# Kernel optimization log

Measured on AMD Instinct MI355X. Metric: run time of the kernel, lower is better.

## Reference

```python
import jax, jax.numpy as jnp
import numpy as np

EMBED_DIM = 1024
NUM_HEADS = 16
HEAD_DIM = EMBED_DIM // NUM_HEADS


def setup_inputs() -> dict:
    key = jax.random.key(0)
    k_x, k_wqkv, k_bqkv, k_wo, k_bo = jax.random.split(key, 5)
    B, T, C = 4, 2048, EMBED_DIM
    # PyTorch Linear default init scale ~ 1/sqrt(fan_in); use small normals
    s = 1.0 / np.sqrt(C)
    return {
        "x": jax.random.normal(k_x, (B, T, C), dtype=jnp.float32),
        "w_qkv": jax.random.normal(k_wqkv, (C, 3 * C), dtype=jnp.float32) * s,
        "b_qkv": jax.random.normal(k_bqkv, (3 * C,), dtype=jnp.float32) * s,
        "w_out": jax.random.normal(k_wo, (C, C), dtype=jnp.float32) * s,
        "b_out": jax.random.normal(k_bo, (C,), dtype=jnp.float32) * s,
    }


def reference(x, w_qkv, b_qkv, w_out, b_out):
    B, T, C = x.shape
    H, D = NUM_HEADS, HEAD_DIM
    qkv = x @ w_qkv + b_qkv                      # (B, T, 3C)
    q, k, v = jnp.split(qkv, 3, axis=-1)
    # (B, H, T, D)
    q = q.reshape(B, T, H, D).transpose(0, 2, 1, 3)
    k = k.reshape(B, T, H, D).transpose(0, 2, 1, 3)
    v = v.reshape(B, T, H, D).transpose(0, 2, 1, 3)
    scores = jnp.einsum("bhqd,bhkd->bhqk", q, k) / jnp.sqrt(jnp.float32(D))
    causal = jnp.tril(jnp.ones((T, T), dtype=bool))  # (T, T)
    scores = jnp.where(causal[None, None, :, :], scores, -jnp.inf)
    attn = jax.nn.softmax(scores, axis=-1)
    out = jnp.einsum("bhqk,bhkd->bhqd", attn, v)  # (B, H, T, D)
    out = out.transpose(0, 2, 1, 3).reshape(B, T, C)
    return out @ w_out + b_out
```

## Files before the change

kernel.cpp:

```cpp
#include <hip/hip_runtime.h>
#include <hip/hip_bf16.h>

#define B_  4
#define T_  2048
#define C_  1024
#define H_  16
#define D_  64
#define BH_ (B_*H_)

typedef float  f32x4  __attribute__((ext_vector_type(4)));
typedef __bf16 bf16x8 __attribute__((ext_vector_type(8)));
typedef __bf16 bf16x2 __attribute__((ext_vector_type(2)));

static __device__ __forceinline__ ushort f2bf(float f) {
    union { float f; unsigned u; } x; x.f = f;
    unsigned r = ((x.u >> 16) & 1u) + 0x7fffu;
    return (ushort)((x.u + r) >> 16);
}

static __device__ __forceinline__ uint packbf(float a, float b) {
    bf16x2 v = { (__bf16)a, (__bf16)b };
    return __builtin_bit_cast(uint, v);
}

static __device__ __forceinline__ void gload_lds16(const void* g, void* l) {
    __builtin_amdgcn_global_load_lds(
        (const __attribute__((address_space(1))) unsigned int*)g,
        (__attribute__((address_space(3))) unsigned int*)l, 16, 0, 0);
}

template<int N> static __device__ __forceinline__ void waitcnt_vm() {
    if constexpr (N == 0) asm volatile("s_waitcnt vmcnt(0)" ::: "memory");
    else if constexpr (N == 3) asm volatile("s_waitcnt vmcnt(3)" ::: "memory");
    else if constexpr (N == 4) asm volatile("s_waitcnt vmcnt(4)" ::: "memory");
    else static_assert(N == 0 || N == 3 || N == 4);
    __builtin_amdgcn_sched_barrier(0);
}
static __device__ __forceinline__ void lgkm0() {
    asm volatile("s_waitcnt lgkmcnt(0)" ::: "memory");
    __builtin_amdgcn_sched_barrier(0);
}

__global__ void cvt_kernel(const float* __restrict__ in, ushort* __restrict__ out, int n) {
    int i = (blockIdx.x * blockDim.x + threadIdx.x) * 4;
    if (i < n) {
        float4 v = *(const float4*)(in + i);
        ushort4 o;
        o.x = f2bf(v.x); o.y = f2bf(v.y); o.z = f2bf(v.z); o.w = f2bf(v.w);
        *(ushort4*)(out + i) = o;
    }
}

__global__ void transpose_cvt_kernel(const float* __restrict__ in, ushort* __restrict__ out,
                                     int K, int N) {
    __shared__ float tile[32][33];
    int k0 = blockIdx.y * 32, n0 = blockIdx.x * 32;
    int tx = threadIdx.x & 31, ty = threadIdx.x >> 5;
    #pragma unroll
    for (int r = 0; r < 32; r += 8)
        tile[ty + r][tx] = in[(size_t)(k0 + ty + r) * N + n0 + tx];
    __syncthreads();
    #pragma unroll
    for (int r = 0; r < 32; r += 8)
        out[(size_t)(n0 + ty + r) * K + k0 + tx] = f2bf(tile[tx][ty + r]);
}

template<int MFR, int NFR, bool QKV>
__global__ __launch_bounds__(512, 2) void gemm_hk(
    const ushort* __restrict__ A,
    const ushort* __restrict__ Bt,
    const float*  __restrict__ bias,
    void* __restrict__ outp,
    ushort* __restrict__ vtp)
{
    constexpr int NT    = 16;
    constexpr int BM    = MFR * 32;
    constexpr int BN    = NFR * 64;
    constexpr int APASS = BM / 128;
    constexpr int LB    = BN / 128;
    constexpr int ABUF  = BM * 128;
    constexpr int BBUF  = BN * 128;
    constexpr int PK    = APASS + LB;
    __shared__ __align__(16) char lds[2 * ABUF + 2 * BBUF];
    char* ldsB = lds + 2 * ABUF;

    const int gX   = gridDim.x;
    const int orig = blockIdx.y * gX + blockIdx.x;
    const int cpx  = (gX * gridDim.y) >> 3;
    const int wg   = (orig & 7) * cpx + (orig >> 3);
    const int m0 = (wg / gX) * BM, n0 = (wg % gX) * BN;

    const int tid = threadIdx.x, lane = tid & 63;
    const int wv = tid >> 6, wm = wv >> 2, wn = wv & 3;
    const int lr = lane & 15, lh = lane >> 4;

    const int sc = (tid & 3) ^ ((tid >> 2) & 3);
    const ushort* aA = A  + (size_t)(m0 + (tid >> 2)) * 1024 + sc * 8;
    const ushort* aB = Bt + (size_t)(n0 + (tid >> 2)) * 1024 + sc * 8;

    const int cxor = (lh ^ (lr & 3)) * 16;
    const int arow = (wm * (MFR * 16) + lr) * 64 + cxor;
    const int brow = (wn * (NFR * 16) + lr) * 64 + cxor;

    f32x4 acc[MFR][NFR] = {};

    auto stage_a = [&](int buf, int t, int kh) {
        #pragma unroll
        for (int p = 0; p < APASS; ++p)
            gload_lds16(aA + (size_t)p * 131072 + t * 64 + kh * 32,
                        lds + buf * ABUF + kh * (ABUF / 2) + p * 8192 + tid * 16);
    };
    auto stage_b = [&](int buf, int t, int kh) {
        #pragma unroll
        for (int p = 0; p < LB; ++p)
            gload_lds16(aB + (size_t)p * 131072 + t * 64 + kh * 32,
                        ldsB + buf * BBUF + kh * (BBUF / 2) + p * 8192 + tid * 16);
    };
    auto read_a = [&](bf16x8 (&af)[MFR], int buf, int kh) {
        const char* base = lds + buf * ABUF + kh * (ABUF / 2) + arow;
        #pragma unroll
        for (int mi = 0; mi < MFR; ++mi) af[mi] = *(const bf16x8*)(base + mi * 1024);
    };
    auto read_b = [&](bf16x8& b0, bf16x8& b1, int buf, int kh, int nh) {
        const char* base = ldsB + buf * BBUF + kh * (BBUF / 2) + brow + nh * 2048;
        b0 = *(const bf16x8*)(base);
        b1 = *(const bf16x8*)(base + 1024);
    };

#define MFMA2(NI, BB0, BB1)                                                          \
    do {                                                                             \
        __builtin_amdgcn_s_setprio(1);                                               \
        _Pragma("unroll")                                                            \
        for (int mi = 0; mi < MFR; ++mi) {                                           \
            acc[mi][NI]     = __builtin_amdgcn_mfma_f32_16x16x32_bf16(af[mi], BB0,   \
                                                     acc[mi][NI], 0, 0, 0);          \
            acc[mi][NI + 1] = __builtin_amdgcn_mfma_f32_16x16x32_bf16(af[mi], BB1,   \
                                                     acc[mi][NI + 1], 0, 0, 0);      \
        }                                                                            \
        __builtin_amdgcn_s_setprio(0);                                               \
    } while (0)

    stage_a(0, 0, 0); stage_b(0, 0, 0);
    stage_a(0, 0, 1); stage_b(0, 0, 1);
    waitcnt_vm<PK>();
    __builtin_amdgcn_s_barrier();

    for (int t = 0; t < NT; ++t) {
        const int cur = t & 1, nxt = cur ^ 1;
        const bool pf = (t + 1 < NT);
        bf16x8 af[MFR], b0, b1;
        if constexpr (NFR == 4) {
            read_a(af, cur, 0); read_b(b0, b1, cur, 0, 0);
            if (pf) stage_a(nxt, t + 1, 0);
            __builtin_amdgcn_s_barrier();
            lgkm0();
            MFMA2(0, b0, b1);
            read_b(b0, b1, cur, 0, 1);
            if (pf) stage_b(nxt, t + 1, 0);
            if (t < NT - 1) waitcnt_vm<PK>(); else waitcnt_vm<0>();
            __builtin_amdgcn_s_barrier();
            lgkm0();
            MFMA2(2, b0, b1);
            read_a(af, cur, 1); read_b(b0, b1, cur, 1, 0);
            if (pf) stage_a(nxt, t + 1, 1);
            __builtin_amdgcn_s_barrier();
            lgkm0();
            MFMA2(0, b0, b1);
            read_b(b0, b1, cur, 1, 1);
            if (pf) stage_b(nxt, t + 1, 1);
            if (t < NT - 1) waitcnt_vm<PK>();
            __builtin_amdgcn_s_barrier();
            lgkm0();
            MFMA2(2, b0, b1);
        } else {
            read_a(af, cur, 0); read_b(b0, b1, cur, 0, 0);
            if (pf) { stage_a(nxt, t + 1, 0); stage_b(nxt, t + 1, 0); }
            if (t < NT - 1) waitcnt_vm<PK>(); else waitcnt_vm<0>();
            __builtin_amdgcn_s_barrier();
            lgkm0();
            MFMA2(0, b0, b1);
            read_a(af, cur, 1); read_b(b0, b1, cur, 1, 0);
            if (pf) { stage_a(nxt, t + 1, 1); stage_b(nxt, t + 1, 1); }
            if (t < NT - 1) waitcnt_vm<PK>();
            __builtin_amdgcn_s_barrier();
            lgkm0();
            MFMA2(0, b0, b1);
        }
    }
#undef MFMA2

    #pragma unroll
    for (int mi = 0; mi < MFR; ++mi) {
        #pragma unroll
        for (int ni = 0; ni < NFR; ++ni) {
            int col = n0 + wn * (NFR * 16) + ni * 16 + lr;
            float bv = bias[col];
            if constexpr (QKV) {
                ushort* qkv = (ushort*)outp;
                int which = col >> 10;
                int h = (col & 1023) >> 6;
                int d = col & 63;
                if (which == 2) {
                    #pragma unroll
                    for (int r = 0; r < 4; ++r) {
                        int row = m0 + wm * (MFR * 16) + mi * 16 + lh * 4 + r;
                        int b = row >> 11, tt = row & 2047;
                        vtp[(((size_t)(b * H_ + h)) * D_ + d) * T_ + tt] =
                            f2bf(acc[mi][ni][r] + bv);
                    }
                } else {
                    #pragma unroll
                    for (int r = 0; r < 4; ++r) {
                        int row = m0 + wm * (MFR * 16) + mi * 16 + lh * 4 + r;
                        int b = row >> 11, tt = row & 2047;
                        float v = acc[mi][ni][r] + bv;
                        if (which == 0) v *= 0.18033688011112042f;
                        qkv[(size_t)which * (BH_ * T_ * D_) +
                            (((size_t)(b * H_ + h)) * T_ + tt) * D_ + d] = f2bf(v);
                    }
                }
            } else {
                float* Cout = (float*)outp;
                #pragma unroll
                for (int r = 0; r < 4; ++r) {
                    int row = m0 + wm * (MFR * 16) + mi * 16 + lh * 4 + r;
                    Cout[(size_t)row * C_ + col] = acc[mi][ni][r] + bv;
                }
            }
        }
    }
}

__global__ __launch_bounds__(256, 5) void flash_kernel(
    const ushort* __restrict__ qb,
    const ushort* __restrict__ kb,
    const ushort* __restrict__ vt,
    ushort* __restrict__ ob)
{
    __shared__ __align__(16) ushort sK[2][64 * 64];
    __shared__ __align__(16) ushort sV[2][64 * 64];
    const int wg  = ((blockIdx.x & 7) << 7) | (blockIdx.x >> 3);
    const int bh  = wg >> 4;
    const int pr  = wg & 15;
    const int qtA = pr, qtB = 31 - pr;
    const int lane = threadIdx.x & 63, wv = threadIdx.x >> 6;
    const int lr = lane & 15, lh = lane >> 4;

    const ushort* qrowA = qb + ((size_t)bh * T_ + qtA * 64 + wv * 16 + lr) * D_;
    const ushort* qrowB = qb + ((size_t)bh * T_ + qtB * 64 + wv * 16 + lr) * D_;
    bf16x8 qfA0 = *(const bf16x8*)(qrowA + lh * 8);
    bf16x8 qfA1 = *(const bf16x8*)(qrowA + 32 + lh * 8);
    bf16x8 qfB0 = *(const bf16x8*)(qrowB + lh * 8);
    bf16x8 qfB1 = *(const bf16x8*)(qrowB + 32 + lh * 8);

    const int srow = lane >> 3;
    const int scol = ((lane & 7) ^ srow) * 8;
    const ushort* kbase = kb + (size_t)bh * T_ * D_;
    const ushort* vbase = vt + (size_t)bh * D_ * T_;

    const int swv  = (lr & 7) << 4;
    const int off0 = (16 * lh) ^ swv;
    const int off1 = (64 + 16 * lh) ^ swv;

    f32x4 oA[4] = {}, oB[4] = {};
    float mA = -1e30f, lA = 0.f, mB = -1e30f, lB = 0.f;

    auto redmax = [&](float x) {
        x = fmaxf(x, __int_as_float(__builtin_amdgcn_ds_swizzle(__float_as_int(x), 0x401F)));
        x = fmaxf(x, __shfl_xor(x, 32, 64));
        return x;
    };
    auto redsum = [&](float x) {
        x += __int_as_float(__builtin_amdgcn_ds_swizzle(__float_as_int(x), 0x401F));
        x += __shfl_xor(x, 32, 64);
        return x;
    };

    auto tile = [&](f32x4 (&o)[4], float& mrow, float& lsum,
                    const bf16x8& q0f, const bf16x8& q1f,
                    const char* K0, const char* V0, bool diag) {
        f32x4 s[4];
        __builtin_amdgcn_s_setprio(1);
        #pragma unroll
        for (int nt = 0; nt < 4; ++nt) {
            const int kk  = ((lr >> 2) << 3) | (lr & 3) | ((nt & 1) << 2) | ((nt >> 1) << 5);
            const int swk = (kk & 7) << 4;
            const char* krow = K0 + kk * 128;
            bf16x8 k0 = *(const bf16x8*)(krow + ((16 * lh) ^ swk));
            bf16x8 k1 = *(const bf16x8*)(krow + ((64 + 16 * lh) ^ swk));
            f32x4 a = {0.f, 0.f, 0.f, 0.f};
            a = __builtin_amdgcn_mfma_f32_16x16x32_bf16(k0, q0f, a, 0, 0, 0);
            a = __builtin_amdgcn_mfma_f32_16x16x32_bf16(k1, q1f, a, 0, 0, 0);
            s[nt] = a;
        }
        __builtin_amdgcn_s_setprio(0);
        if (diag) {
            #pragma unroll
            for (int nt = 0; nt < 4; ++nt) {
                const int kb0 = 8 * lh + 4 * (nt & 1) + 32 * (nt >> 1);
                #pragma unroll
                for (int r = 0; r < 4; ++r)
                    if (kb0 + r > wv * 16 + lr) s[nt][r] = -INFINITY;
            }
        }

        float pmax = fmaxf(fmaxf(fmaxf(s[0][0], s[0][1]), fmaxf(s[0][2], s[0][3])),
                           fmaxf(fmaxf(s[1][0], s[1][1]), fmaxf(s[1][2], s[1][3])));
        pmax = fmaxf(pmax, fmaxf(fmaxf(fmaxf(s[2][0], s[2][1]), fmaxf(s[2][2], s[2][3])),
                                 fmaxf(fmaxf(s[3][0], s[3][1]), fmaxf(s[3][2], s[3][3]))));
        pmax = redmax(pmax);

        if (__any(pmax > mrow + 8.f)) {
            float mnew = fmaxf(mrow, pmax);
            float al = __builtin_exp2f(mrow - mnew);
            lsum *= al;
            #pragma unroll
            for (int r = 0; r < 4; ++r) {
                float ar = __shfl(al, lh * 20 + r, 64);
                o[0][r] *= ar; o[1][r] *= ar; o[2][r] *= ar; o[3][r] *= ar;
            }
            mrow = mnew;
        }

        float rsum = 0.f;
        uint pk[8];
        #pragma unroll
        for (int nt = 0; nt < 4; ++nt) {
            float p0 = __builtin_exp2f(s[nt][0] - mrow);
            float p1 = __builtin_exp2f(s[nt][1] - mrow);
            float p2 = __builtin_exp2f(s[nt][2] - mrow);
            float p3 = __builtin_exp2f(s[nt][3] - mrow);
            rsum += (p0 + p1) + (p2 + p3);
            pk[nt * 2]     = packbf(p0, p1);
            pk[nt * 2 + 1] = packbf(p2, p3);
        }
        lsum += redsum(rsum);

        uint4 w0 = {pk[0], pk[1], pk[2], pk[3]};
        uint4 w1 = {pk[4], pk[5], pk[6], pk[7]};
        bf16x8 pf0 = __builtin_bit_cast(bf16x8, w0);
        bf16x8 pf1 = __builtin_bit_cast(bf16x8, w1);

        __builtin_amdgcn_s_setprio(1);
        #pragma unroll
        for (int dt = 0; dt < 4; ++dt) {
            const char* vrow = V0 + (dt * 16 + lr) * 128;
            bf16x8 v0 = *(const bf16x8*)(vrow + off0);
            bf16x8 v1 = *(const bf16x8*)(vrow + off1);
            o[dt] = __builtin_amdgcn_mfma_f32_16x16x32_bf16(pf0, v0, o[dt], 0, 0, 0);
            o[dt] = __builtin_amdgcn_mfma_f32_16x16x32_bf16(pf1, v1, o[dt], 0, 0, 0);
        }
        __builtin_amdgcn_s_setprio(0);
    };

    #pragma unroll
    for (int i = 0; i < 2; ++i) {
        int j = i * 4 + wv;
        gload_lds16(kbase + (size_t)(j * 8 + srow) * D_ + scol, &sK[0][j * 512]);
        gload_lds16(vbase + (size_t)(j * 8 + srow) * T_ + scol, &sV[0][j * 512]);
    }
    __syncthreads();

    for (int kt = 0; kt <= qtB; ++kt) {
        const int cur = kt & 1;
        if (kt < qtB) {
            const int nb = cur ^ 1;
            #pragma unroll
            for (int i = 0; i < 2; ++i) {
                int j = i * 4 + wv;
                gload_lds16(kbase + (size_t)((kt + 1) * 64 + j * 8 + srow) * D_ + scol, &sK[nb][j * 512]);
                gload_lds16(vbase + (size_t)(j * 8 + srow) * T_ + (kt + 1) * 64 + scol, &sV[nb][j * 512]);
            }
        }
        const char* K0 = (const char*)sK[cur];
        const char* V0 = (const char*)sV[cur];
        if (kt <= qtA) tile(oA, mA, lA, qfA0, qfA1, K0, V0, kt == qtA);
        tile(oB, mB, lB, qfB0, qfB1, K0, V0, kt == qtB);
        __syncthreads();
    }

    const int b = bh >> 4, h = bh & 15;
    auto writeout = [&](f32x4 (&o)[4], float lsum, int q0) {
        float inv = 1.f / lsum;
        #pragma unroll
        for (int r = 0; r < 4; ++r) {
            float ir = __shfl(inv, lh * 20 + r, 64);
            int q = q0 + lh * 4 + r;
            #pragma unroll
            for (int dt = 0; dt < 4; ++dt)
                ob[((size_t)b * T_ + q) * C_ + h * 64 + dt * 16 + lr] = f2bf(o[dt][r] * ir);
        }
    };
    writeout(oA, lA, qtA * 64 + wv * 16);
    writeout(oB, lB, qtB * 64 + wv * 16);
}

extern "C" void kernel_launch(void* const* d_in, const int* in_sizes, int n_in,
                              void* d_out, int out_size, void* d_ws, size_t ws_size,
                              hipStream_t stream) {
    const float* x     = (const float*)d_in[0];
    const float* w_qkv = (const float*)d_in[1];
    const float* b_qkv = (const float*)d_in[2];
    const float* w_out = (const float*)d_in[3];
    const float* b_out = (const float*)d_in[4];
    float* out = (float*)d_out;

    char* ws = (char*)d_ws;
    ushort* xb     = (ushort*)(ws + 0);
    ushort* wqkvT  = (ushort*)(ws + 16777216);
    ushort* woutT  = (ushort*)(ws + 23068672);
    ushort* qkv    = (ushort*)(ws + 25165824);
    ushort* vT     = (ushort*)(ws + 75497472);
    ushort* attn   = xb;
    ushort* qb = qkv;
    ushort* kb = qkv + (size_t)BH_ * T_ * D_;

    const int nx = B_ * T_ * C_;
    cvt_kernel<<<nx / 4 / 256, 256, 0, stream>>>(x, xb, nx);
    transpose_cvt_kernel<<<dim3(3 * C_ / 32, C_ / 32), 256, 0, stream>>>(w_qkv, wqkvT, C_, 3 * C_);
    transpose_cvt_kernel<<<dim3(C_ / 32, C_ / 32), 256, 0, stream>>>(w_out, woutT, C_, C_);
    gemm_hk<4, 4, true><<<dim3(3 * C_ / 256, B_ * T_ / 128), 512, 0, stream>>>(xb, wqkvT, b_qkv, qkv, vT);
    flash_kernel<<<BH_ * 16, 256, 0, stream>>>(qb, kb, vT, attn);
    gemm_hk<8, 2, false><<<dim3(C_ / 128, B_ * T_ / 256), 512, 0, stream>>>(attn, woutT, b_out, out, nullptr);
}
```

Before: 210.2 us.

## Share K fragment reads across both query tiles and retile QKV GEMM

The flash kernel now computes QK^T scores for both query tiles (A and B) in one loop, so each K fragment read from LDS is reused for two MFMA chains instead of being loaded twice. The two softmax/PV phases then run afterward. The occupancy hint drops from 5 to 4 to allow more registers for the extra live score tiles. The QKV GEMM switches from the 4x4 fragment config to the 8x2 config, which lets the NFR==4 pipelined path be removed. More live registers may cost occupancy, and the new QKV tile shape changes the grid.

Measured after the change: 199.2 us. 5.3% less time.

```diff
diff --git a/kernel.cpp b/kernel.cpp
--- a/kernel.cpp
+++ b/kernel.cpp
@@ -149,43 +149,18 @@
         const int cur = t & 1, nxt = cur ^ 1;
         const bool pf = (t + 1 < NT);
         bf16x8 af[MFR], b0, b1;
-        if constexpr (NFR == 4) {
-            read_a(af, cur, 0); read_b(b0, b1, cur, 0, 0);
-            if (pf) stage_a(nxt, t + 1, 0);
-            __builtin_amdgcn_s_barrier();
-            lgkm0();
-            MFMA2(0, b0, b1);
-            read_b(b0, b1, cur, 0, 1);
-            if (pf) stage_b(nxt, t + 1, 0);
-            if (t < NT - 1) waitcnt_vm<PK>(); else waitcnt_vm<0>();
-            __builtin_amdgcn_s_barrier();
-            lgkm0();
-            MFMA2(2, b0, b1);
-            read_a(af, cur, 1); read_b(b0, b1, cur, 1, 0);
-            if (pf) stage_a(nxt, t + 1, 1);
-            __builtin_amdgcn_s_barrier();
-            lgkm0();
-            MFMA2(0, b0, b1);
-            read_b(b0, b1, cur, 1, 1);
-            if (pf) stage_b(nxt, t + 1, 1);
-            if (t < NT - 1) waitcnt_vm<PK>();
-            __builtin_amdgcn_s_barrier();
-            lgkm0();
-            MFMA2(2, b0, b1);
-        } else {
-            read_a(af, cur, 0); read_b(b0, b1, cur, 0, 0);
-            if (pf) { stage_a(nxt, t + 1, 0); stage_b(nxt, t + 1, 0); }
-            if (t < NT - 1) waitcnt_vm<PK>(); else waitcnt_vm<0>();
-            __builtin_amdgcn_s_barrier();
-            lgkm0();
-            MFMA2(0, b0, b1);
-            read_a(af, cur, 1); read_b(b0, b1, cur, 1, 0);
-            if (pf) { stage_a(nxt, t + 1, 1); stage_b(nxt, t + 1, 1); }
-            if (t < NT - 1) waitcnt_vm<PK>();
-            __builtin_amdgcn_s_barrier();
-            lgkm0();
-            MFMA2(0, b0, b1);
-        }
+        read_a(af, cur, 0); read_b(b0, b1, cur, 0, 0);
+        if (pf) { stage_a(nxt, t + 1, 0); stage_b(nxt, t + 1, 0); }
+        if (t < NT - 1) waitcnt_vm<PK>(); else waitcnt_vm<0>();
+        __builtin_amdgcn_s_barrier();
+        lgkm0();
+        MFMA2(0, b0, b1);
+        read_a(af, cur, 1); read_b(b0, b1, cur, 1, 0);
+        if (pf) { stage_a(nxt, t + 1, 1); stage_b(nxt, t + 1, 1); }
+        if (t < NT - 1) waitcnt_vm<PK>();
+        __builtin_amdgcn_s_barrier();
+        lgkm0();
+        MFMA2(0, b0, b1);
     }
 #undef MFMA2
 
@@ -231,7 +206,7 @@
     }
 }
 
-__global__ __launch_bounds__(256, 5) void flash_kernel(
+__global__ __launch_bounds__(256, 4) void flash_kernel(
     const ushort* __restrict__ qb,
     const ushort* __restrict__ kb,
     const ushort* __restrict__ vt,
@@ -276,40 +251,23 @@
         return x;
     };
 
-    auto tile = [&](f32x4 (&o)[4], float& mrow, float& lsum,
-                    const bf16x8& q0f, const bf16x8& q1f,
-                    const char* K0, const char* V0, bool diag) {
-        f32x4 s[4];
-        __builtin_amdgcn_s_setprio(1);
+    auto maskS = [&](f32x4 (&s)[4]) {
         #pragma unroll
         for (int nt = 0; nt < 4; ++nt) {
-            const int kk  = ((lr >> 2) << 3) | (lr & 3) | ((nt & 1) << 2) | ((nt >> 1) << 5);
-            const int swk = (kk & 7) << 4;
-            const char* krow = K0 + kk * 128;
-            bf16x8 k0 = *(const bf16x8*)(krow + ((16 * lh) ^ swk));
-            bf16x8 k1 = *(const bf16x8*)(krow + ((64 + 16 * lh) ^ swk));
-            f32x4 a = {0.f, 0.f, 0.f, 0.f};
-            a = __builtin_amdgcn_mfma_f32_16x16x32_bf16(k0, q0f, a, 0, 0, 0);
-            a = __builtin_amdgcn_mfma_f32_16x16x32_bf16(k1, q1f, a, 0, 0, 0);
-            s[nt] = a;
-        }
-        __builtin_amdgcn_s_setprio(0);
-        if (diag) {
+            const int kb0 = 8 * lh + 4 * (nt & 1) + 32 * (nt >> 1);
             #pragma unroll
-            for (int nt = 0; nt < 4; ++nt) {
-                const int kb0 = 8 * lh + 4 * (nt & 1) + 32 * (nt >> 1);
-                #pragma unroll
-                for (int r = 0; r < 4; ++r)
-                    if (kb0 + r > wv * 16 + lr) s[nt][r] = -INFINITY;
-            }
-        }
-
+            for (int r = 0; r < 4; ++r)
+                if (kb0 + r > wv * 16 + lr) s[nt][r] = -INFINITY;
+        }
+    };
+
+    auto softmax_pv = [&](f32x4 (&s)[4], float& mrow, float& lsum, f32x4 (&o)[4],
+                          const char* V0) {
         float pmax = fmaxf(fmaxf(fmaxf(s[0][0], s[0][1]), fmaxf(s[0][2], s[0][3])),
                            fmaxf(fmaxf(s[1][0], s[1][1]), fmaxf(s[1][2], s[1][3])));
         pmax = fmaxf(pmax, fmaxf(fmaxf(fmaxf(s[2][0], s[2][1]), fmaxf(s[2][2], s[2][3])),
                                  fmaxf(fmaxf(s[3][0], s[3][1]), fmaxf(s[3][2], s[3][3]))));
         pmax = redmax(pmax);
-
         if (__any(pmax > mrow + 8.f)) {
             float mnew = fmaxf(mrow, pmax);
             float al = __builtin_exp2f(mrow - mnew);
@@ -321,7 +279,6 @@
             }
             mrow = mnew;
         }
-
         float rsum = 0.f;
         uint pk[8];
         #pragma unroll
@@ -335,12 +292,10 @@
             pk[nt * 2 + 1] = packbf(p2, p3);
         }
         lsum += redsum(rsum);
-
         uint4 w0 = {pk[0], pk[1], pk[2], pk[3]};
         uint4 w1 = {pk[4], pk[5], pk[6], pk[7]};
         bf16x8 pf0 = __builtin_bit_cast(bf16x8, w0);
         bf16x8 pf1 = __builtin_bit_cast(bf16x8, w1);
-
         __builtin_amdgcn_s_setprio(1);
         #pragma unroll
         for (int dt = 0; dt < 4; ++dt) {
@@ -372,10 +327,36 @@
                 gload_lds16(vbase + (size_t)(j * 8 + srow) * T_ + (kt + 1) * 64 + scol, &sV[nb][j * 512]);
             }
         }
+        const bool doA = kt <= qtA;
         const char* K0 = (const char*)sK[cur];
         const char* V0 = (const char*)sV[cur];
-        if (kt <= qtA) tile(oA, mA, lA, qfA0, qfA1, K0, V0, kt == qtA);
-        tile(oB, mB, lB, qfB0, qfB1, K0, V0, kt == qtB);
+
+        f32x4 sa[4], sb[4];
+        __builtin_amdgcn_s_setprio(1);
+        #pragma unroll
+        for (int nt = 0; nt < 4; ++nt) {
+            const int kk  = ((lr >> 2) << 3) | (lr & 3) | ((nt & 1) << 2) | ((nt >> 1) << 5);
+            const int swk = (kk & 7) << 4;
+            const char* krow = K0 + kk * 128;
+            bf16x8 k0 = *(const bf16x8*)(krow + ((16 * lh) ^ swk));
+            bf16x8 k1 = *(const bf16x8*)(krow + ((64 + 16 * lh) ^ swk));
+            f32x4 a = {0.f, 0.f, 0.f, 0.f};
+            a = __builtin_amdgcn_mfma_f32_16x16x32_bf16(k0, qfB0, a, 0, 0, 0);
+            a = __builtin_amdgcn_mfma_f32_16x16x32_bf16(k1, qfB1, a, 0, 0, 0);
+            sb[nt] = a;
+            if (doA) {
+                f32x4 c = {0.f, 0.f, 0.f, 0.f};
+                c = __builtin_amdgcn_mfma_f32_16x16x32_bf16(k0, qfA0, c, 0, 0, 0);
+                c = __builtin_amdgcn_mfma_f32_16x16x32_bf16(k1, qfA1, c, 0, 0, 0);
+                sa[nt] = c;
+            }
+        }
+        __builtin_amdgcn_s_setprio(0);
+        if (kt == qtB) maskS(sb);
+        if (doA && kt == qtA) maskS(sa);
+
+        softmax_pv(sb, mB, lB, oB, V0);
+        if (doA) softmax_pv(sa, mA, lA, oA, V0);
         __syncthreads();
     }
 
@@ -419,7 +400,7 @@
     cvt_kernel<<<nx / 4 / 256, 256, 0, stream>>>(x, xb, nx);
     transpose_cvt_kernel<<<dim3(3 * C_ / 32, C_ / 32), 256, 0, stream>>>(w_qkv, wqkvT, C_, 3 * C_);
     transpose_cvt_kernel<<<dim3(C_ / 32, C_ / 32), 256, 0, stream>>>(w_out, woutT, C_, C_);
-    gemm_hk<4, 4, true><<<dim3(3 * C_ / 256, B_ * T_ / 128), 512, 0, stream>>>(xb, wqkvT, b_qkv, qkv, vT);
+    gemm_hk<8, 2, true><<<dim3(3 * C_ / 128, B_ * T_ / 256), 512, 0, stream>>>(xb, wqkvT, b_qkv, qkv, vT);
     flash_kernel<<<BH_ * 16, 256, 0, stream>>>(qb, kb, vT, attn);
     gemm_hk<8, 2, false><<<dim3(C_ / 128, B_ * T_ / 256), 512, 0, stream>>>(attn, woutT, b_out, out, nullptr);
 }
```
